# Performance work log

Measured on AMD Instinct MI355X. Metric: run time of the kernel, lower is better.

## Reference

```python
import jax, jax.numpy as jnp
import numpy as np

# QuantizedLinear (BitNet-style ternary weights).
# The original pack_weights/unpack_weights 2-bit round-trip is an identity on the
# ternary values; the nested-loop ternary_matrix_operation is mathematically
# x @ Q^T (weights stored [out, in], accumulating +x[:,i] / -x[:,i] per +-1 entry).

def setup_inputs() -> dict:
    key = jax.random.key(0)
    k1, k2 = jax.random.split(key)
    TOKENS, IN_F, OUT_F = 8192, 4096, 4096
    x = jax.random.normal(k1, (TOKENS, IN_F), dtype=jnp.float32)
    weight = jax.random.normal(k2, (OUT_F, IN_F), dtype=jnp.float32)
    bias = jnp.zeros((OUT_F,), dtype=jnp.float32)
    return {"x": x, "weight": weight, "bias": bias}

def reference(x, weight, bias):
    # absmean ternary quantization: gamma = mean(|W|) + eps
    gamma = jnp.mean(jnp.abs(weight)) + 1e-5
    q = jnp.clip(jnp.round(weight / gamma), -1.0, 1.0)  # ternary {-1,0,1}, [out,in]
    # pack->unpack 2-bit round-trip is identity; loop accumulation == GEMM
    return jnp.einsum('bi,oi->bo', x, q) + bias
```

## Files before the change

### kernel.cpp

```cpp
#include <hip/hip_runtime.h>
#include <stdint.h>


#define M_DIM 8192
#define N_DIM 4096
#define K_DIM 4096
#define BM 256
#define BN 256
#define BK 64

typedef __attribute__((ext_vector_type(4))) int vi4;

#define BAR() asm volatile("s_barrier" ::: "memory")
#define VMW0() asm volatile("s_waitcnt vmcnt(0)" ::: "memory")
#define VMW4() asm volatile("s_waitcnt vmcnt(4)" ::: "memory")
#define SB0() __builtin_amdgcn_sched_barrier(0)
#define LGKM(n)                                             \
  do {                                                      \
    SB0();                                                  \
    asm volatile("s_waitcnt lgkmcnt(" #n ")" ::: "memory"); \
    SB0();                                                  \
  } while (0)

__device__ __forceinline__ void load_lds16(const void* g, void* l) {
  __builtin_amdgcn_global_load_lds(
      (const __attribute__((address_space(1))) void*)g,
      (__attribute__((address_space(3))) void*)l,
      16, 0, 0);
}

__global__ __launch_bounds__(256) void k_abs_partial(const float* __restrict__ w,
                                                     double* __restrict__ partial) {
  const int tid = threadIdx.x;
  const size_t base = (size_t)blockIdx.x * 8192 + (size_t)tid * 4;
  double s = 0.0;
#pragma unroll
  for (int it = 0; it < 8; ++it) {
    const float4 v = *reinterpret_cast<const float4*>(w + base + (size_t)it * 1024);
    s += (double)fabsf(v.x) + (double)fabsf(v.y) + (double)fabsf(v.z) + (double)fabsf(v.w);
  }
  __shared__ double sd[256];
  sd[tid] = s;
  __syncthreads();
  for (int off = 128; off > 0; off >>= 1) {
    if (tid < off) sd[tid] += sd[tid + off];
    __syncthreads();
  }
  if (tid == 0) partial[blockIdx.x] = sd[0];
}

__global__ __launch_bounds__(256) void k_abs_final(const double* __restrict__ partial,
                                                   float* __restrict__ gamma_out) {
  const int tid = threadIdx.x;
  double s = 0.0;
  for (int i = tid; i < 2048; i += 256) s += partial[i];
  __shared__ double sd[256];
  sd[tid] = s;
  __syncthreads();
  for (int off = 128; off > 0; off >>= 1) {
    if (tid < off) sd[tid] += sd[tid + off];
    __syncthreads();
  }
  if (tid == 0) {
    float g = (float)(sd[0] / 16777216.0);
    gamma_out[0] = g + 1e-5f;
  }
}

__global__ __launch_bounds__(256) void k_quant(const float* __restrict__ w,
                                               const float* __restrict__ gamma_p,
                                               int* __restrict__ qb) {
  const float g = gamma_p[0];
  const size_t n4 = (size_t)N_DIM * K_DIM / 4;
  const size_t stride = (size_t)gridDim.x * blockDim.x;
  for (size_t i = (size_t)blockIdx.x * blockDim.x + threadIdx.x; i < n4; i += stride) {
    const float4 v = reinterpret_cast<const float4*>(w)[i];
    float r;
    int a, b, c, d;
    r = rintf(v.x / g); a = (r >= 1.0f) ? 1 : ((r <= -1.0f) ? -1 : 0);
    r = rintf(v.y / g); b = (r >= 1.0f) ? 1 : ((r <= -1.0f) ? -1 : 0);
    r = rintf(v.z / g); c = (r >= 1.0f) ? 1 : ((r <= -1.0f) ? -1 : 0);
    r = rintf(v.w / g); d = (r >= 1.0f) ? 1 : ((r <= -1.0f) ? -1 : 0);
    qb[i] = (a & 0xff) | ((b & 0xff) << 8) | ((c & 0xff) << 16) | ((d & 0xff) << 24);
  }
}

__global__ __launch_bounds__(256) void k_quant_x(const float* __restrict__ x,
                                                 signed char* __restrict__ xq,
                                                 float* __restrict__ xs) {
  const int row = blockIdx.x;
  const int tid = threadIdx.x;
  const float* xr = x + (size_t)row * K_DIM;
  float4 v[4];
  float am = 0.0f;
#pragma unroll
  for (int i = 0; i < 4; ++i) {
    v[i] = reinterpret_cast<const float4*>(xr)[tid * 4 + i];
    am = fmaxf(am, fmaxf(fmaxf(fabsf(v[i].x), fabsf(v[i].y)),
                         fmaxf(fabsf(v[i].z), fabsf(v[i].w))));
  }
  for (int off = 32; off > 0; off >>= 1) am = fmaxf(am, __shfl_down(am, off));
  __shared__ float sm[4];
  if ((tid & 63) == 0) sm[tid >> 6] = am;
  __syncthreads();
  const float bm = fmaxf(fmaxf(fmaxf(sm[0], sm[1]), fmaxf(sm[2], sm[3])), 1e-20f);
  if (tid == 0) xs[row] = bm / 127.0f;
  const float inv = 127.0f / bm;
  union { signed char c[16]; int4 q; } u;
#pragma unroll
  for (int i = 0; i < 4; ++i) {
    u.c[i * 4 + 0] = (signed char)(int)rintf(v[i].x * inv);
    u.c[i * 4 + 1] = (signed char)(int)rintf(v[i].y * inv);
    u.c[i * 4 + 2] = (signed char)(int)rintf(v[i].z * inv);
    u.c[i * 4 + 3] = (signed char)(int)rintf(v[i].w * inv);
  }
  *reinterpret_cast<int4*>(xq + (size_t)row * K_DIM + tid * 16) = u.q;
}

__global__ __launch_bounds__(512, 2) void k_gemm(const signed char* __restrict__ Aq,
                                                 const signed char* __restrict__ Bq,
                                                 const float* __restrict__ xs,
                                                 const float* __restrict__ bias,
                                                 float* __restrict__ C) {
  __shared__ unsigned char lds[2][2][256][64];

  const int tid = threadIdx.x;
  const int wid = tid >> 6;
  const int lane = tid & 63;
  const int wm = wid >> 2;
  const int wn = wid & 3;
  const int l15 = lane & 15;
  const int l4 = lane >> 4;

  const int brow = blockIdx.y * BM;
  const int bcol = blockIdx.x * BN;

  const int srow = wid * 16 + (lane >> 2);
  const int scol = ((lane & 3) ^ ((lane >> 3) & 3)) << 4;
  const int rdoff = ((l4 ^ ((l15 >> 1) & 3)) << 4);

#define STAGE1(buf, op, half, kt)                                                  \
  do {                                                                             \
    const signed char* g =                                                         \
        ((op) ? Bq + (size_t)(bcol + (half)*128 + srow) * K_DIM                    \
              : Aq + (size_t)(brow + (half)*128 + srow) * K_DIM) + (kt)*64 + scol; \
    load_lds16(g, (char*)&lds[buf][op][(half)*128][0] + (size_t)wid * 1024);       \
  } while (0)
#define STAGE_ALL(buf, kt)       \
  do {                           \
    STAGE1(buf, 0, 0, kt);       \
    STAGE1(buf, 0, 1, kt);       \
    STAGE1(buf, 1, 0, kt);       \
    STAGE1(buf, 1, 1, kt);       \
  } while (0)

#define READ_SET(AR, BR, buf)                                                     \
  do {                                                                            \
    _Pragma("unroll") for (int i = 0; i < 8; ++i)                                 \
      AR[i] = *reinterpret_cast<const vi4*>(                                      \
          &lds[buf][0][0][0] + (size_t)(wm * 128 + i * 16 + l15) * 64 + rdoff);   \
    _Pragma("unroll") for (int p = 0; p < 4; ++p)                                 \
      BR[p] = *reinterpret_cast<const vi4*>(                                      \
          &lds[buf][1][0][0] + (size_t)(p * 64 + wn * 16 + l15) * 64 + rdoff);    \
    SB0();                                                                        \
  } while (0)

#define MFMA32(AR, BR)                                                            \
  do {                                                                            \
    __builtin_amdgcn_s_setprio(1);                                                \
    _Pragma("unroll") for (int i = 0; i < 8; ++i)                                 \
      _Pragma("unroll") for (int p = 0; p < 4; ++p)                               \
        acc[i][p] = __builtin_amdgcn_mfma_i32_16x16x64_i8(AR[i], BR[p],           \
                                                          acc[i][p], 0, 0, 0);    \
    __builtin_amdgcn_s_setprio(0);                                                \
  } while (0)

  vi4 acc[8][4];
#pragma unroll
  for (int i = 0; i < 8; ++i)
#pragma unroll
    for (int p = 0; p < 4; ++p)
#pragma unroll
      for (int e = 0; e < 4; ++e) acc[i][p][e] = 0;

  vi4 Aa[8], Ba[4], Ab[8], Bb[4];

  STAGE_ALL(0, 0);
  STAGE_ALL(1, 1);
  VMW4();
  BAR();
  READ_SET(Aa, Ba, 0);

  for (int tp = 0; tp < 31; ++tp) {
    const int t = 2 * tp;
    VMW0();
    BAR();
    READ_SET(Ab, Bb, 1);
    LGKM(12);
    STAGE_ALL(0, t + 2);
    MFMA32(Aa, Ba);
    VMW0();
    BAR();
    READ_SET(Aa, Ba, 0);
    LGKM(12);
    STAGE_ALL(1, t + 3);
    MFMA32(Ab, Bb);
  }
  VMW0();
  BAR();
  READ_SET(Ab, Bb, 1);
  LGKM(12);
  MFMA32(Aa, Ba);
  LGKM(0);
  MFMA32(Ab, Bb);

  float bi[4];
#pragma unroll
  for (int p = 0; p < 4; ++p) bi[p] = bias[bcol + p * 64 + wn * 16 + l15];
#pragma unroll
  for (int i = 0; i < 8; ++i) {
#pragma unroll
    for (int j = 0; j < 4; ++j) {
      const int row = brow + wm * 128 + i * 16 + l4 * 4 + j;
      const float sc = xs[row];
      float* crow = C + (size_t)row * N_DIM + bcol + wn * 16 + l15;
#pragma unroll
      for (int p = 0; p < 4; ++p) crow[p * 64] = (float)acc[i][p][j] * sc + bi[p];
    }
  }
#undef STAGE1
#undef STAGE_ALL
#undef READ_SET
#undef MFMA32
}

extern "C" void kernel_launch(void* const* d_in, const int* in_sizes, int n_in,
                              void* d_out, int out_size, void* d_ws, size_t ws_size,
                              hipStream_t stream) {
  (void)in_sizes; (void)n_in; (void)out_size; (void)ws_size;
  const float* x = (const float*)d_in[0];
  const float* w = (const float*)d_in[1];
  const float* bias = (const float*)d_in[2];
  float* out = (float*)d_out;

  char* ws = (char*)d_ws;
  signed char* xq = (signed char*)ws;
  signed char* qb = (signed char*)(ws + (size_t)M_DIM * K_DIM);
  float* xs = (float*)(ws + (size_t)M_DIM * K_DIM + (size_t)N_DIM * K_DIM);
  double* partial = (double*)((char*)xs + M_DIM * sizeof(float));
  float* gamma = (float*)(partial + 2048);

  k_abs_partial<<<2048, 256, 0, stream>>>(w, partial);
  k_abs_final<<<1, 256, 0, stream>>>(partial, gamma);
  k_quant<<<2048, 256, 0, stream>>>(w, gamma, (int*)qb);
  k_quant_x<<<M_DIM, 256, 0, stream>>>(x, xq, xs);

  dim3 grid(N_DIM / BN, M_DIM / BM);
  k_gemm<<<grid, 512, 0, stream>>>(xq, qb, xs, bias, out);
}
```

Measured before the change: 199.2 us.

## Triple-buffer LDS with split-half MFMA schedule and XCD-aware block swizzle

Rewrites the int8 GEMM main loop to use three LDS stages instead of two. Each k-step is split into two quarter-tile MFMA phases, with the global-to-LDS loads for the A and B halves interleaved between them, so loads and compute overlap more finely. A 1D grid with a swizzle groups column tiles by blockIdx modulo 8 to improve L2 locality across XCDs. LDS use grows to 96KB per block, which may limit two blocks per CU, and the loop now has more barriers.

```diff
diff --git a/kernel.cpp b/kernel.cpp
--- a/kernel.cpp
+++ b/kernel.cpp
@@ -12,13 +12,13 @@
 typedef __attribute__((ext_vector_type(4))) int vi4;
 
 #define BAR() asm volatile("s_barrier" ::: "memory")
+#define VMW4() asm volatile("s_waitcnt vmcnt(4)" ::: "memory")
 #define VMW0() asm volatile("s_waitcnt vmcnt(0)" ::: "memory")
-#define VMW4() asm volatile("s_waitcnt vmcnt(4)" ::: "memory")
 #define SB0() __builtin_amdgcn_sched_barrier(0)
-#define LGKM(n)                                             \
+#define LGKM0()                                             \
   do {                                                      \
     SB0();                                                  \
-    asm volatile("s_waitcnt lgkmcnt(" #n ")" ::: "memory"); \
+    asm volatile("s_waitcnt lgkmcnt(0)" ::: "memory");      \
     SB0();                                                  \
   } while (0)
 
@@ -122,7 +122,7 @@
                                                  const float* __restrict__ xs,
                                                  const float* __restrict__ bias,
                                                  float* __restrict__ C) {
-  __shared__ unsigned char lds[2][2][256][64];
+  __shared__ unsigned char lds[3][2][256][64];
 
   const int tid = threadIdx.x;
   const int wid = tid >> 6;
@@ -132,8 +132,10 @@
   const int l15 = lane & 15;
   const int l4 = lane >> 4;
 
-  const int brow = blockIdx.y * BM;
-  const int bcol = blockIdx.x * BN;
+  const int c8 = blockIdx.x & 7;
+  const int idx = blockIdx.x >> 3;
+  const int bcol = (c8 * 2 + (idx & 1)) * BN;
+  const int brow = (idx >> 1) * BM;
 
   const int srow = wid * 16 + (lane >> 2);
   const int scol = ((lane & 3) ^ ((lane >> 3) & 3)) << 4;
@@ -146,34 +148,21 @@
               : Aq + (size_t)(brow + (half)*128 + srow) * K_DIM) + (kt)*64 + scol; \
     load_lds16(g, (char*)&lds[buf][op][(half)*128][0] + (size_t)wid * 1024);       \
   } while (0)
-#define STAGE_ALL(buf, kt)       \
-  do {                           \
-    STAGE1(buf, 0, 0, kt);       \
-    STAGE1(buf, 0, 1, kt);       \
-    STAGE1(buf, 1, 0, kt);       \
-    STAGE1(buf, 1, 1, kt);       \
-  } while (0)
-
-#define READ_SET(AR, BR, buf)                                                     \
-  do {                                                                            \
-    _Pragma("unroll") for (int i = 0; i < 8; ++i)                                 \
-      AR[i] = *reinterpret_cast<const vi4*>(                                      \
-          &lds[buf][0][0][0] + (size_t)(wm * 128 + i * 16 + l15) * 64 + rdoff);   \
-    _Pragma("unroll") for (int p = 0; p < 4; ++p)                                 \
-      BR[p] = *reinterpret_cast<const vi4*>(                                      \
-          &lds[buf][1][0][0] + (size_t)(p * 64 + wn * 16 + l15) * 64 + rdoff);    \
-    SB0();                                                                        \
-  } while (0)
-
-#define MFMA32(AR, BR)                                                            \
-  do {                                                                            \
-    __builtin_amdgcn_s_setprio(1);                                                \
-    _Pragma("unroll") for (int i = 0; i < 8; ++i)                                 \
-      _Pragma("unroll") for (int p = 0; p < 4; ++p)                               \
-        acc[i][p] = __builtin_amdgcn_mfma_i32_16x16x64_i8(AR[i], BR[p],           \
-                                                          acc[i][p], 0, 0, 0);    \
-    __builtin_amdgcn_s_setprio(0);                                                \
-  } while (0)
+
+#define RD_A(AR, buf, i0)                                                         \
+  _Pragma("unroll") for (int i = 0; i < 4; ++i)                                   \
+    AR[i] = *reinterpret_cast<const vi4*>(                                        \
+        &lds[buf][0][0][0] + (size_t)(wm * 128 + ((i0) + i) * 16 + l15) * 64 + rdoff);
+#define RD_B(BR, buf, p0)                                                         \
+  _Pragma("unroll") for (int p = 0; p < 2; ++p)                                   \
+    BR[p] = *reinterpret_cast<const vi4*>(                                        \
+        &lds[buf][1][0][0] + (size_t)(((p0) + p) * 64 + wn * 16 + l15) * 64 + rdoff);
+
+#define MFMAQ(AV, BV, IO, PO)                                                     \
+  _Pragma("unroll") for (int i = 0; i < 4; ++i)                                   \
+    _Pragma("unroll") for (int p = 0; p < 2; ++p)                                 \
+      acc[(IO) + i][(PO) + p] = __builtin_amdgcn_mfma_i32_16x16x64_i8(            \
+          AV[i], BV[p], acc[(IO) + i][(PO) + p], 0, 0, 0);
 
   vi4 acc[8][4];
 #pragma unroll
@@ -183,36 +172,51 @@
 #pragma unroll
       for (int e = 0; e < 4; ++e) acc[i][p][e] = 0;
 
-  vi4 Aa[8], Ba[4], Ab[8], Bb[4];
-
-  STAGE_ALL(0, 0);
-  STAGE_ALL(1, 1);
+  vi4 aL[4], aH[4], bL[2], bH[2];
+
+  STAGE1(0, 0, 0, 0); STAGE1(0, 0, 1, 0); STAGE1(0, 1, 0, 0); STAGE1(0, 1, 1, 0);
+  STAGE1(1, 0, 0, 1); STAGE1(1, 0, 1, 1); STAGE1(1, 1, 0, 1); STAGE1(1, 1, 1, 1);
   VMW4();
   BAR();
-  READ_SET(Aa, Ba, 0);
-
-  for (int tp = 0; tp < 31; ++tp) {
-    const int t = 2 * tp;
-    VMW0();
-    BAR();
-    READ_SET(Ab, Bb, 1);
-    LGKM(12);
-    STAGE_ALL(0, t + 2);
-    MFMA32(Aa, Ba);
-    VMW0();
-    BAR();
-    READ_SET(Aa, Ba, 0);
-    LGKM(12);
-    STAGE_ALL(1, t + 3);
-    MFMA32(Ab, Bb);
-  }
-  VMW0();
-  BAR();
-  READ_SET(Ab, Bb, 1);
-  LGKM(12);
-  MFMA32(Aa, Ba);
-  LGKM(0);
-  MFMA32(Ab, Bb);
+
+  int cur = 0;
+  for (int t = 0; t < 63; ++t) {
+    const int stg = (cur == 0) ? 2 : cur - 1;
+    RD_A(aL, cur, 0);
+    RD_B(bL, cur, 0);
+    SB0();
+    if (t < 62) { STAGE1(stg, 0, 0, t + 2); STAGE1(stg, 0, 1, t + 2); }
+    BAR();
+    LGKM0();
+    __builtin_amdgcn_s_setprio(1);
+    MFMAQ(aL, bL, 0, 0);
+    __builtin_amdgcn_s_setprio(0);
+    BAR();
+    RD_A(aH, cur, 4);
+    RD_B(bH, cur, 2);
+    SB0();
+    if (t < 62) { STAGE1(stg, 1, 0, t + 2); STAGE1(stg, 1, 1, t + 2); }
+    BAR();
+    LGKM0();
+    __builtin_amdgcn_s_setprio(1);
+    MFMAQ(aH, bH, 4, 2);
+    MFMAQ(aL, bH, 0, 2);
+    MFMAQ(aH, bL, 4, 0);
+    __builtin_amdgcn_s_setprio(0);
+    if (t < 62) VMW4(); else VMW0();
+    BAR();
+    cur = (cur == 2) ? 0 : cur + 1;
+  }
+
+  RD_A(aL, cur, 0); RD_B(bL, cur, 0);
+  RD_A(aH, cur, 4); RD_B(bH, cur, 2);
+  LGKM0();
+  __builtin_amdgcn_s_setprio(1);
+  MFMAQ(aL, bL, 0, 0);
+  MFMAQ(aH, bH, 4, 2);
+  MFMAQ(aL, bH, 0, 2);
+  MFMAQ(aH, bL, 4, 0);
+  __builtin_amdgcn_s_setprio(0);
 
   float bi[4];
 #pragma unroll
@@ -229,9 +233,9 @@
     }
   }
 #undef STAGE1
-#undef STAGE_ALL
-#undef READ_SET
-#undef MFMA32
+#undef RD_A
+#undef RD_B
+#undef MFMAQ
 }
 
 extern "C" void kernel_launch(void* const* d_in, const int* in_sizes, int n_in,
@@ -255,6 +259,5 @@
   k_quant<<<2048, 256, 0, stream>>>(w, gamma, (int*)qb);
   k_quant_x<<<M_DIM, 256, 0, stream>>>(x, xq, xs);
 
-  dim3 grid(N_DIM / BN, M_DIM / BM);
-  k_gemm<<<grid, 512, 0, stream>>>(xq, qb, xs, bias, out);
-}
+  k_gemm<<<512, 512, 0, stream>>>(xq, qb, xs, bias, out);
+}
```

After: 202.9 us. No clear change (+1.9%).
